# Optimization experiments

Measured on AMD Instinct MI355X. Metric: run time of the kernel, lower is better.

## Reference

```python
import jax, jax.numpy as jnp
import numpy as np

# Model hyperparameters (upscaled from the repo's shakespear config)
L, E, H, T, B, V = 6, 1024, 16, 1024, 4, 32000
HD = E // H          # head_size = 64
EPS = 1e-5


def layernorm(x, g, b):
    m = x.mean(-1, keepdims=True)
    v = ((x - m) ** 2).mean(-1, keepdims=True)
    return (x - m) / jnp.sqrt(v + EPS) * g + b


def setup_inputs() -> dict:
    key = jax.random.key(0)
    ks = jax.random.split(key, 24)
    s = 0.02
    n = lambda k, shp: (jax.random.normal(k, shp) * s).astype(jnp.float32)
    return {
        "idx": jax.random.randint(ks[0], (B, T), 0, V),
        "tok_emb": n(ks[1], (V, E)),
        "pos_emb": n(ks[2], (T, E)),
        # per-head q/k/v weights stacked: [L, E, H, HD]
        "Wq": n(ks[3], (L, E, H, HD)),
        "Wk": n(ks[4], (L, E, H, HD)),
        "Wv": n(ks[5], (L, E, H, HD)),
        "Wo": n(ks[6], (L, E, E)),
        "bo": jnp.zeros((L, E), jnp.float32),
        "W1": n(ks[7], (L, E, 4 * E)),
        "b1": jnp.zeros((L, 4 * E), jnp.float32),
        "W2": n(ks[8], (L, 4 * E, E)),
        "b2": jnp.zeros((L, E), jnp.float32),
        "ln1_g": jnp.ones((L, E), jnp.float32),
        "ln1_b": jnp.zeros((L, E), jnp.float32),
        "ln2_g": jnp.ones((L, E), jnp.float32),
        "ln2_b": jnp.zeros((L, E), jnp.float32),
        "lnf_g": jnp.ones((E,), jnp.float32),
        "lnf_b": jnp.zeros((E,), jnp.float32),
        "Wlm": n(ks[9], (E, V)),
        "blm": jnp.zeros((V,), jnp.float32),
    }


def reference(idx, tok_emb, pos_emb, Wq, Wk, Wv, Wo, bo, W1, b1, W2, b2,
              ln1_g, ln1_b, ln2_g, ln2_b, lnf_g, lnf_b, Wlm, blm):
    x = tok_emb[idx] + pos_emb[None, :T]            # [B,T,E]
    mask = jnp.tril(jnp.ones((T, T), bool))
    scale = HD ** -0.5
    for l in range(L):
        h = layernorm(x, ln1_g[l], ln1_b[l])
        q = jnp.einsum('bte,ehd->bhtd', h, Wq[l])
        k = jnp.einsum('bte,ehd->bhtd', h, Wk[l])
        v = jnp.einsum('bte,ehd->bhtd', h, Wv[l])
        # NOTE: source computes K @ Q^T (reversed from standard attention)
        wei = jnp.einsum('bhtd,bhsd->bhts', k, q) * scale
        wei = jnp.where(mask, wei, -jnp.inf)
        wei = jax.nn.softmax(wei, axis=-1)
        att = jnp.einsum('bhts,bhsd->bhtd', wei, v)  # [B,H,T,HD]
        att = att.transpose(0, 2, 1, 3).reshape(B, T, E)
        x = x + att @ Wo[l] + bo[l]
        h2 = layernorm(x, ln2_g[l], ln2_b[l])
        x = x + jax.nn.relu(h2 @ W1[l] + b1[l]) @ W2[l] + b2[l]
    x = layernorm(x, lnf_g, lnf_b)
    logits = x @ Wlm + blm                           # [B,T,V]
    return logits
```

## Files before the change

kernel.cpp:

```cpp
#include <hip/hip_runtime.h>


typedef __bf16 bf16;
typedef __attribute__((ext_vector_type(8))) __bf16 bf16x8;
typedef __attribute__((ext_vector_type(4))) __bf16 bf16x4;
typedef __attribute__((ext_vector_type(4))) float  f32x4;

#define LAYERS 6
#define EMB    1024
#define HEADS  16
#define HDIM   64
#define SEQ    1024
#define BATCH  4
#define VOCAB  32000
#define ROWS   (BATCH * SEQ)

#define AS1(p) ((__attribute__((address_space(1))) void*)(p))
#define AS3(p) ((__attribute__((address_space(3))) void*)(p))

__global__ void transpose_cvt(const float* __restrict__ in, bf16* __restrict__ out,
                              int K, int N)
{
    __shared__ float tile[32][33];
    int n0 = blockIdx.x * 32, k0 = blockIdx.y * 32;
    int tx = threadIdx.x, ty = threadIdx.y;
#pragma unroll
    for (int r = 0; r < 4; ++r)
        tile[ty + 8 * r][tx] = in[(size_t)(k0 + ty + 8 * r) * N + n0 + tx];
    __syncthreads();
#pragma unroll
    for (int r = 0; r < 4; ++r)
        out[(size_t)(n0 + ty + 8 * r) * K + k0 + tx] = (bf16)tile[tx][ty + 8 * r];
}

__global__ void transpose_all(const float* __restrict__ Wq, const float* __restrict__ Wk,
                              const float* __restrict__ Wv, const float* __restrict__ Wo,
                              const float* __restrict__ W1, const float* __restrict__ W2,
                              bf16* __restrict__ Tq, bf16* __restrict__ Tk,
                              bf16* __restrict__ Tv, bf16* __restrict__ To,
                              bf16* __restrict__ T1, bf16* __restrict__ T2)
{
    __shared__ float tile[32][33];
    int tx = threadIdx.x, ty = threadIdx.y;
    int id = blockIdx.x;
    const float* in; bf16* out; int K, N, n0, k0;
    if (id < 4096) {
        int z = id >> 10, rem = id & 1023;
        int bx = rem & 31, by = rem >> 5;
        K = 1024; N = 1024; n0 = bx * 32; k0 = by * 32;
        switch (z) {
            case 0: in = Wq; out = Tq; break;
            case 1: in = Wk; out = Tk; break;
            case 2: in = Wv; out = Tv; break;
            default: in = Wo; out = To; break;
        }
    } else if (id < 8192) {
        int rem = id - 4096;
        int bx = rem & 127, by = rem >> 7;
        in = W1; out = T1; K = 1024; N = 4096; n0 = bx * 32; k0 = by * 32;
    } else {
        int rem = id - 8192;
        int bx = rem & 127, by = rem >> 7;
        in = W2; out = T2; K = 4096; N = 1024; n0 = by * 32; k0 = bx * 32;
    }
#pragma unroll
    for (int r = 0; r < 4; ++r)
        tile[ty + 8 * r][tx] = in[(size_t)(k0 + ty + 8 * r) * N + n0 + tx];
    __syncthreads();
#pragma unroll
    for (int r = 0; r < 4; ++r)
        out[(size_t)(n0 + ty + 8 * r) * K + k0 + tx] = (bf16)tile[tx][ty + 8 * r];
}

__global__ void embed_kernel(const int* __restrict__ idx, const float* __restrict__ tok,
                             const float* __restrict__ pos, bf16* __restrict__ x)
{
    int row = blockIdx.x;
    int t   = row & (SEQ - 1);
    int id  = idx[row];
    int e   = threadIdx.x;
    float4 a = ((const float4*)(tok + (size_t)id * EMB))[e];
    float4 p = ((const float4*)(pos + (size_t)t  * EMB))[e];
    bf16x4 o;
    o.x = (bf16)(a.x + p.x); o.y = (bf16)(a.y + p.y);
    o.z = (bf16)(a.z + p.z); o.w = (bf16)(a.w + p.w);
    *(bf16x4*)(x + (size_t)row * EMB + e * 4) = o;
}

__global__ __launch_bounds__(256)
void ln_kernel(const bf16* __restrict__ x, const float* __restrict__ g,
               const float* __restrict__ b, bf16* __restrict__ out)
{
    int row = blockIdx.x;
    int t = threadIdx.x;
    bf16x4 xv = *(const bf16x4*)(x + (size_t)row * EMB + t * 4);
    float4 v; v.x = (float)xv.x; v.y = (float)xv.y; v.z = (float)xv.z; v.w = (float)xv.w;
    float s1 = v.x + v.y + v.z + v.w;
    float s2 = v.x * v.x + v.y * v.y + v.z * v.z + v.w * v.w;
#pragma unroll
    for (int off = 32; off > 0; off >>= 1) {
        s1 += __shfl_down(s1, off);
        s2 += __shfl_down(s2, off);
    }
    __shared__ float l1[4], l2[4];
    int wave = t >> 6;
    if ((t & 63) == 0) { l1[wave] = s1; l2[wave] = s2; }
    __syncthreads();
    float tot1 = l1[0] + l1[1] + l1[2] + l1[3];
    float tot2 = l2[0] + l2[1] + l2[2] + l2[3];
    float mean = tot1 * (1.f / EMB);
    float var  = tot2 * (1.f / EMB) - mean * mean;
    float rstd = rsqrtf(var + 1e-5f);
    float4 gg = ((const float4*)g)[t];
    float4 bb = ((const float4*)b)[t];
    bf16x4 o;
    o.x = (bf16)((v.x - mean) * rstd * gg.x + bb.x);
    o.y = (bf16)((v.y - mean) * rstd * gg.y + bb.y);
    o.z = (bf16)((v.z - mean) * rstd * gg.z + bb.z);
    o.w = (bf16)((v.w - mean) * rstd * gg.w + bb.w);
    *(bf16x4*)(out + (size_t)row * EMB + t * 4) = o;
}

template <int MODE>
__global__ __launch_bounds__(512, 1)
void gemm256_kernel(const bf16* __restrict__ A, const bf16* __restrict__ BT,
                    void* Cv, const float* __restrict__ bias,
                    int N, int K, int nbm, int nbn)
{
    __shared__ __align__(16) bf16 lds[2][2][256 * 64];
    const int tid  = threadIdx.x;
    const int wave = tid >> 6, lane = tid & 63;
    const int lo = lane & 15, hi = lane >> 4;
    const int wm = wave >> 2, wn = wave & 3;

    const int nwg = nbm * nbn;
    const int q = nwg >> 3, rem = nwg & 7;
    const int xcd = blockIdx.x & 7, boff = blockIdx.x >> 3;
    const int swz = (xcd < rem ? xcd * (q + 1) : rem * (q + 1) + (xcd - rem) * q) + boff;
    const int m0 = (swz % nbm) * 256;
    const int n0 = (swz / nbm) * 256;

    f32x4 acc[8][4];
#pragma unroll
    for (int m = 0; m < 8; ++m)
#pragma unroll
        for (int n = 0; n < 4; ++n)
            acc[m][n] = (f32x4){0.f, 0.f, 0.f, 0.f};

    const int NT = K >> 6;

    auto stage_ht = [&](int t, int ht) {
        const int slot = t & 1;
        const int k0 = t << 6;
        const int ab = ht >> 1;
        const int rbase = (ht & 1) << 7;
        const bf16* src = ab ? BT : A;
        const int base0 = ab ? n0 : m0;
#pragma unroll
        for (int j = 0; j < 2; ++j) {
            int g  = j * 512 + tid;
            int r  = g >> 3;
            int cc = (g & 7) ^ (r & 7);
            __builtin_amdgcn_global_load_lds(
                AS1(src + (size_t)(base0 + rbase + r) * K + k0 + cc * 8),
                AS3((char*)&lds[slot][ab][rbase * 64] + (size_t)g * 16), 16, 0, 0);
        }
    };

    bf16x8 bcur[4][2], bnxt[4][2], ae[2][2], ao[2][2];

    auto lda = [&](int t, int mp, bf16x8 (&out)[2][2]) {
        const int slot = t & 1;
#pragma unroll
        for (int mi = 0; mi < 2; ++mi)
#pragma unroll
            for (int ks = 0; ks < 2; ++ks) {
                int r = wm * 128 + (mp * 2 + mi) * 16 + lo;
                int pos = (ks * 4 + hi) ^ (r & 7);
                out[mi][ks] = *(const bf16x8*)(&lds[slot][0][r * 64 + pos * 8]);
            }
    };
    auto ldb = [&](int t, bf16x8 (&out)[4][2]) {
        const int slot = t & 1;
#pragma unroll
        for (int n = 0; n < 4; ++n)
#pragma unroll
            for (int ks = 0; ks < 2; ++ks) {
                int r = wn * 64 + n * 16 + lo;
                int pos = (ks * 4 + hi) ^ (r & 7);
                out[n][ks] = *(const bf16x8*)(&lds[slot][1][r * 64 + pos * 8]);
            }
    };
    auto mfma16 = [&](int mp, bf16x8 (&a)[2][2]) {
        __builtin_amdgcn_s_setprio(1);
#pragma unroll
        for (int mi = 0; mi < 2; ++mi)
#pragma unroll
            for (int n = 0; n < 4; ++n)
#pragma unroll
                for (int ks = 0; ks < 2; ++ks)
                    acc[mp * 2 + mi][n] =
                        __builtin_amdgcn_mfma_f32_16x16x32_bf16(a[mi][ks], bcur[n][ks],
                                                                acc[mp * 2 + mi][n], 0, 0, 0);
        __builtin_amdgcn_s_setprio(0);
    };

    stage_ht(0, 0); stage_ht(0, 1); stage_ht(0, 2); stage_ht(0, 3);
    asm volatile("s_waitcnt vmcnt(0)\n\ts_barrier" ::: "memory");
    ldb(0, bcur);
    lda(0, 0, ae);

    for (int t = 0; t < NT; ++t) {
        const bool more = (t + 1 < NT);
        if (more) { stage_ht(t + 1, 0); stage_ht(t + 1, 1); }
        lda(t, 1, ao);
        mfma16(0, ae);
        if (more) { stage_ht(t + 1, 2); stage_ht(t + 1, 3); }
        lda(t, 2, ae);
        mfma16(1, ao);
        lda(t, 3, ao);
        mfma16(2, ae);
        if (more) {
            asm volatile("s_waitcnt vmcnt(0) lgkmcnt(0)\n\ts_barrier" ::: "memory");
            ldb(t + 1, bnxt);
            lda(t + 1, 0, ae);
        }
        mfma16(3, ao);
        if (more) {
#pragma unroll
            for (int n = 0; n < 4; ++n)
#pragma unroll
                for (int ks = 0; ks < 2; ++ks)
                    bcur[n][ks] = bnxt[n][ks];
        }
    }

#pragma unroll
    for (int m = 0; m < 8; ++m) {
        int row = m0 + wm * 128 + m * 16 + hi * 4;
#pragma unroll
        for (int n = 0; n < 4; ++n) {
            int col = n0 + wn * 64 + n * 16 + lo;
            float bv = (MODE != 0) ? bias[col] : 0.f;
#pragma unroll
            for (int j = 0; j < 4; ++j) {
                size_t o = (size_t)(row + j) * N + col;
                float v = acc[m][n][j] + bv;
                if (MODE == 2)      ((bf16*)Cv)[o]  = (bf16)fmaxf(v, 0.f);
                else if (MODE == 3) ((float*)Cv)[o] = v;
                else                ((bf16*)Cv)[o]  = (bf16)v;
            }
        }
    }
}

template <int MODE>
__global__ __launch_bounds__(256)
void gemm_kernel(const bf16* __restrict__ A, const bf16* __restrict__ BT,
                 void* Cv, const float* __restrict__ bias,
                 const bf16* __restrict__ resid, bf16* __restrict__ vt,
                 int N, int K)
{
    __shared__ __align__(16) bf16 As[128 * 64];
    __shared__ __align__(16) bf16 Bs[128 * 64];
    const int tid = threadIdx.x;
    const int wave = tid >> 6, lane = tid & 63;
    const int lo = lane & 15, hi = lane >> 4;
    const int wm = wave >> 1, wn = wave & 1;
    const int m0 = blockIdx.y * 128, n0 = blockIdx.x * 128;

    f32x4 acc[4][4];
#pragma unroll
    for (int m = 0; m < 4; ++m)
#pragma unroll
        for (int n = 0; n < 4; ++n)
            acc[m][n] = (f32x4){0.f, 0.f, 0.f, 0.f};

    const int sb = wave * 4;
    for (int k0 = 0; k0 < K; k0 += 64) {
#pragma unroll
        for (int i = 0; i < 4; ++i) {
            int g   = (sb + i) * 64 + lane;
            int row = g >> 3;
            int lc  = (g & 7) ^ (row & 7);
            const bf16* ga = A  + (size_t)(m0 + row) * K + k0 + lc * 8;
            const bf16* gb = BT + (size_t)(n0 + row) * K + k0 + lc * 8;
            __builtin_amdgcn_global_load_lds(AS1(ga), AS3(As + (sb + i) * 512), 16, 0, 0);
            __builtin_amdgcn_global_load_lds(AS1(gb), AS3(Bs + (sb + i) * 512), 16, 0, 0);
        }
        asm volatile("s_waitcnt vmcnt(0)" ::: "memory");
        __syncthreads();
#pragma unroll
        for (int ks = 0; ks < 2; ++ks) {
            bf16x8 af[4], bfr[4];
#pragma unroll
            for (int m = 0; m < 4; ++m) {
                int r  = wm * 64 + m * 16 + lo;
                int pc = (ks * 4 + hi) ^ (r & 7);
                af[m] = *(const bf16x8*)(As + r * 64 + pc * 8);
            }
#pragma unroll
            for (int n = 0; n < 4; ++n) {
                int r  = wn * 64 + n * 16 + lo;
                int pc = (ks * 4 + hi) ^ (r & 7);
                bfr[n] = *(const bf16x8*)(Bs + r * 64 + pc * 8);
            }
#pragma unroll
            for (int m = 0; m < 4; ++m)
#pragma unroll
                for (int n = 0; n < 4; ++n)
                    acc[m][n] = __builtin_amdgcn_mfma_f32_16x16x32_bf16(af[m], bfr[n], acc[m][n], 0, 0, 0);
        }
        __syncthreads();
    }

    if (MODE == 4 && n0 >= 2048) {
#pragma unroll
        for (int m = 0; m < 4; ++m) {
            int rowb = m0 + wm * 64 + m * 16 + hi * 4;
            int bb = rowb >> 10, t = rowb & 1023;
#pragma unroll
            for (int n = 0; n < 4; ++n) {
                int hd = n0 - 2048 + wn * 64 + n * 16 + lo;
                bf16x4 w;
                w.x = (bf16)acc[m][n][0]; w.y = (bf16)acc[m][n][1];
                w.z = (bf16)acc[m][n][2]; w.w = (bf16)acc[m][n][3];
                *(bf16x4*)(vt + ((size_t)(bb * 1024 + hd)) * SEQ + t) = w;
            }
        }
        return;
    }

#pragma unroll
    for (int m = 0; m < 4; ++m) {
        int rbase = m0 + wm * 64 + m * 16 + hi * 4;
#pragma unroll
        for (int n = 0; n < 4; ++n) {
            int col = n0 + wn * 64 + n * 16 + lo;
            float bv = (MODE == 1) ? bias[col] : 0.f;
#pragma unroll
            for (int j = 0; j < 4; ++j) {
                size_t off = (size_t)(rbase + j) * N + col;
                float v = acc[m][n][j] + bv;
                if (MODE == 1)      ((bf16*)Cv)[off] = (bf16)(v + (float)resid[off]);
                else                ((bf16*)Cv)[off] = (bf16)v;
            }
        }
    }
}

template <int MODE>
__global__ __launch_bounds__(256)
void gemm64_kernel(const bf16* __restrict__ A, const bf16* __restrict__ BT,
                   bf16* __restrict__ C, const float* __restrict__ bias,
                   const bf16* __restrict__ resid, int N, int K)
{
    __shared__ __align__(16) bf16 As[64 * 64];
    __shared__ __align__(16) bf16 Bs[128 * 64];
    const int tid = threadIdx.x;
    const int wave = tid >> 6, lane = tid & 63;
    const int lo = lane & 15, hi = lane >> 4;
    const int wm = wave >> 1, wn = wave & 1;
    const int m0 = blockIdx.y * 64, n0 = blockIdx.x * 128;

    f32x4 acc[2][4];
#pragma unroll
    for (int m = 0; m < 2; ++m)
#pragma unroll
        for (int n = 0; n < 4; ++n)
            acc[m][n] = (f32x4){0.f, 0.f, 0.f, 0.f};

    for (int k0 = 0; k0 < K; k0 += 64) {
#pragma unroll
        for (int i = 0; i < 2; ++i) {
            int c   = i * 256 + tid;
            int row = c >> 3;
            int cc  = (c & 7) ^ (row & 7);
            __builtin_amdgcn_global_load_lds(
                AS1(A + (size_t)(m0 + row) * K + k0 + cc * 8),
                AS3(As + (size_t)c * 8), 16, 0, 0);
        }
#pragma unroll
        for (int i = 0; i < 4; ++i) {
            int c   = i * 256 + tid;
            int row = c >> 3;
            int cc  = (c & 7) ^ (row & 7);
            __builtin_amdgcn_global_load_lds(
                AS1(BT + (size_t)(n0 + row) * K + k0 + cc * 8),
                AS3(Bs + (size_t)c * 8), 16, 0, 0);
        }
        asm volatile("s_waitcnt vmcnt(0)" ::: "memory");
        __syncthreads();
#pragma unroll
        for (int ks = 0; ks < 2; ++ks) {
            bf16x8 af[2], bfr[4];
#pragma unroll
            for (int m = 0; m < 2; ++m) {
                int r  = wm * 32 + m * 16 + lo;
                int pc = (ks * 4 + hi) ^ (r & 7);
                af[m] = *(const bf16x8*)(As + r * 64 + pc * 8);
            }
#pragma unroll
            for (int n = 0; n < 4; ++n) {
                int r  = wn * 64 + n * 16 + lo;
                int pc = (ks * 4 + hi) ^ (r & 7);
                bfr[n] = *(const bf16x8*)(Bs + r * 64 + pc * 8);
            }
#pragma unroll
            for (int m = 0; m < 2; ++m)
#pragma unroll
                for (int n = 0; n < 4; ++n)
                    acc[m][n] = __builtin_amdgcn_mfma_f32_16x16x32_bf16(af[m], bfr[n], acc[m][n], 0, 0, 0);
        }
        __syncthreads();
    }

#pragma unroll
    for (int m = 0; m < 2; ++m) {
        int rbase = m0 + wm * 32 + m * 16 + hi * 4;
#pragma unroll
        for (int n = 0; n < 4; ++n) {
            int col = n0 + wn * 64 + n * 16 + lo;
            float bv = bias[col];
#pragma unroll
            for (int j = 0; j < 4; ++j) {
                size_t off = (size_t)(rbase + j) * N + col;
                float v = acc[m][n][j] + bv;
                if (MODE == 1) C[off] = (bf16)(v + (float)resid[off]);
                else           C[off] = (bf16)fmaxf(v, 0.f);
            }
        }
    }
}

__global__ __launch_bounds__(64)
void attn_kernel(const bf16* __restrict__ qkv, const bf16* __restrict__ vt,
                 bf16* __restrict__ att)
{
    int bh = blockIdx.x; int b = bh >> 4, h = bh & 15;
    int t0 = blockIdx.y * 16;
    int lane = threadIdx.x;
    int lo = lane & 15, hi = lane >> 4;
    const bf16* kb = qkv + (size_t)(b * SEQ) * 3072 + EMB + h * 64;
    const bf16* qb = qkv + (size_t)(b * SEQ) * 3072 + h * 64;
    const bf16* vb = vt + (size_t)bh * 64 * SEQ;

    bf16x8 bK0 = *(const bf16x8*)(kb + (size_t)(t0 + lo) * 3072 + hi * 8);
    bf16x8 bK1 = *(const bf16x8*)(kb + (size_t)(t0 + lo) * 3072 + 32 + hi * 8);

    f32x4 o[4];
#pragma unroll
    for (int n = 0; n < 4; ++n) o[n] = (f32x4){0.f, 0.f, 0.f, 0.f};
    float mrun = -1e30f, lrun = 0.f;

    __shared__ __align__(16) bf16 plds[16][72];

    const int nt = (t0 + 16 + 63) >> 6;
    const int nfull = (t0 >= 64) ? (((t0 - 63) >> 6) + 1) : 0;

    auto tile_body = [&](int s0, bool masked) {
        f32x4 sc[4];
#pragma unroll
        for (int sh = 0; sh < 4; ++sh) sc[sh] = (f32x4){0.f, 0.f, 0.f, 0.f};
#pragma unroll
        for (int sh = 0; sh < 4; ++sh) {
            const bf16* qr = qb + (size_t)(s0 + sh * 16 + lo) * 3072;
            bf16x8 aQ0 = *(const bf16x8*)(qr + hi * 8);
            bf16x8 aQ1 = *(const bf16x8*)(qr + 32 + hi * 8);
            sc[sh] = __builtin_amdgcn_mfma_f32_16x16x32_bf16(aQ0, bK0, sc[sh], 0, 0, 0);
            sc[sh] = __builtin_amdgcn_mfma_f32_16x16x32_bf16(aQ1, bK1, sc[sh], 0, 0, 0);
        }
        const int tt = t0 + lo;
        float p[16];
        float mx = -1e30f;
#pragma unroll
        for (int sh = 0; sh < 4; ++sh)
#pragma unroll
            for (int j = 0; j < 4; ++j) {
                float val = sc[sh][j] * 0.125f;
                if (masked) {
                    int s = s0 + sh * 16 + hi * 4 + j;
                    if (s > tt) val = -1e30f;
                }
                p[sh * 4 + j] = val;
                mx = fmaxf(mx, val);
            }
        mx = fmaxf(mx, __shfl_xor(mx, 16));
        mx = fmaxf(mx, __shfl_xor(mx, 32));
        if (__any(mx > mrun + 8.f)) {
            float mnew = fmaxf(mrun, mx);
            float scl = __expf(mrun - mnew);
            mrun = mnew;
            lrun *= scl;
            float sclj[4];
#pragma unroll
            for (int j = 0; j < 4; ++j) sclj[j] = __shfl(scl, hi * 4 + j);
#pragma unroll
            for (int n = 0; n < 4; ++n)
#pragma unroll
                for (int j = 0; j < 4; ++j)
                    o[n][j] *= sclj[j];
        }
        float rs = 0.f;
#pragma unroll
        for (int i = 0; i < 16; ++i) { p[i] = __expf(p[i] - mrun); rs += p[i]; }
        rs += __shfl_xor(rs, 16);
        rs += __shfl_xor(rs, 32);
        lrun += rs;
        __syncthreads();
#pragma unroll
        for (int sh = 0; sh < 4; ++sh) {
            bf16x4 w;
            w.x = (bf16)p[sh * 4 + 0]; w.y = (bf16)p[sh * 4 + 1];
            w.z = (bf16)p[sh * 4 + 2]; w.w = (bf16)p[sh * 4 + 3];
            *(bf16x4*)(&plds[lo][sh * 16 + hi * 4]) = w;
        }
        __syncthreads();
        bf16x8 aP0 = *(const bf16x8*)(&plds[lo][hi * 8]);
        bf16x8 aP1 = *(const bf16x8*)(&plds[lo][32 + hi * 8]);
#pragma unroll
        for (int n = 0; n < 4; ++n) {
            bf16x8 bV0 = *(const bf16x8*)(vb + (size_t)(n * 16 + lo) * SEQ + s0 + hi * 8);
            bf16x8 bV1 = *(const bf16x8*)(vb + (size_t)(n * 16 + lo) * SEQ + s0 + 32 + hi * 8);
            o[n] = __builtin_amdgcn_mfma_f32_16x16x32_bf16(aP0, bV0, o[n], 0, 0, 0);
            o[n] = __builtin_amdgcn_mfma_f32_16x16x32_bf16(aP1, bV1, o[n], 0, 0, 0);
        }
    };

    for (int it = 0; it < nfull; ++it) tile_body(it * 64, false);
    for (int it = nfull; it < nt; ++it) tile_body(it * 64, true);

    float lj[4];
#pragma unroll
    for (int j = 0; j < 4; ++j) lj[j] = __shfl(lrun, hi * 4 + j);
#pragma unroll
    for (int j = 0; j < 4; ++j) {
        float inv = 1.f / lj[j];
        size_t rowoff = (size_t)(b * SEQ + t0 + hi * 4 + j) * EMB + h * 64;
#pragma unroll
        for (int n = 0; n < 4; ++n)
            att[rowoff + n * 16 + lo] = (bf16)(o[n][j] * inv);
    }
}

extern "C" void kernel_launch(void* const* d_in, const int* in_sizes, int n_in,
                              void* d_out, int out_size, void* d_ws, size_t ws_size,
                              hipStream_t stream)
{
    const int*   idx  = (const int*)d_in[0];
    const float* tok  = (const float*)d_in[1];
    const float* pos  = (const float*)d_in[2];
    const float* Wq   = (const float*)d_in[3];
    const float* Wk   = (const float*)d_in[4];
    const float* Wv   = (const float*)d_in[5];
    const float* Wo   = (const float*)d_in[6];
    const float* bo   = (const float*)d_in[7];
    const float* W1   = (const float*)d_in[8];
    const float* b1   = (const float*)d_in[9];
    const float* W2   = (const float*)d_in[10];
    const float* b2   = (const float*)d_in[11];
    const float* ln1g = (const float*)d_in[12];
    const float* ln1b = (const float*)d_in[13];
    const float* ln2g = (const float*)d_in[14];
    const float* ln2b = (const float*)d_in[15];
    const float* lnfg = (const float*)d_in[16];
    const float* lnfb = (const float*)d_in[17];
    const float* Wlm  = (const float*)d_in[18];
    const float* blm  = (const float*)d_in[19];
    float* out = (float*)d_out;

    char* ws = (char*)d_ws;
    size_t off = 0;
    auto alloc = [&](size_t bytes) { void* p = ws + off; off += (bytes + 255) & ~(size_t)255; return p; };
    bf16* x     = (bf16*)alloc((size_t)ROWS * EMB * 2);
    bf16* h     = (bf16*)alloc((size_t)ROWS * EMB * 2);
    bf16* qkv   = (bf16*)alloc((size_t)ROWS * 3072 * 2);
    bf16* vt    = (bf16*)alloc((size_t)ROWS * EMB * 2);
    bf16* attb  = (bf16*)alloc((size_t)ROWS * EMB * 2);
    bf16* mlp   = (bf16*)alloc((size_t)ROWS * 4096 * 2);
    bf16* WTqkv = (bf16*)alloc((size_t)3072 * 1024 * 2);
    bf16* WTo   = (bf16*)alloc((size_t)1024 * 1024 * 2);
    bf16* WT1   = (bf16*)alloc((size_t)4096 * 1024 * 2);
    bf16* WT2   = (bf16*)alloc((size_t)1024 * 4096 * 2);
    bf16* WTlm  = (bf16*)alloc((size_t)VOCAB * 1024 * 2);

    dim3 tb(32, 8);

    transpose_cvt<<<dim3(VOCAB / 32, 32), tb, 0, stream>>>(Wlm, WTlm, 1024, VOCAB);

    embed_kernel<<<ROWS, 256, 0, stream>>>(idx, tok, pos, x);

    for (int l = 0; l < LAYERS; ++l) {
        const size_t wqs = (size_t)l * 1024 * 1024;
        const size_t w14 = (size_t)l * 4096 * 1024;
        transpose_all<<<12288, tb, 0, stream>>>(
            Wq + wqs, Wk + wqs, Wv + wqs, Wo + wqs, W1 + w14, W2 + w14,
            WTqkv, WTqkv + (size_t)1024 * 1024, WTqkv + (size_t)2048 * 1024, WTo,
            WT1, WT2);

        ln_kernel<<<ROWS, 256, 0, stream>>>(x, ln1g + l * EMB, ln1b + l * EMB, h);
        gemm_kernel<4><<<dim3(24, 32), 256, 0, stream>>>(h, WTqkv, qkv, nullptr, nullptr, vt, 3072, 1024);
        attn_kernel<<<dim3(64, 64), 64, 0, stream>>>(qkv, vt, attb);
        gemm64_kernel<1><<<dim3(8, 64), 256, 0, stream>>>(attb, WTo, x, bo + l * EMB, x, 1024, 1024);
        ln_kernel<<<ROWS, 256, 0, stream>>>(x, ln2g + l * EMB, ln2b + l * EMB, h);
        gemm64_kernel<2><<<dim3(32, 64), 256, 0, stream>>>(h, WT1, mlp, b1 + l * 4096, nullptr, 4096, 1024);
        gemm64_kernel<1><<<dim3(8, 64), 256, 0, stream>>>(mlp, WT2, x, b2 + l * EMB, x, 1024, 4096);
    }
    ln_kernel<<<ROWS, 256, 0, stream>>>(x, lnfg, lnfb, h);
    gemm256_kernel<3><<<16 * 125, 512, 0, stream>>>(h, WTlm, out, blm, 32000, 1024, 16, 125);
}
```

Measured before the change: 1.910 ms.

## Process 32 query rows per attention wave and use 256-tile GEMM for MLP up-projection

The attention kernel now handles two 16-row groups per 64-thread block, so each loaded Q tile and V tile feeds twice as many MFMAs, and the grid is halved. The online-softmax rescale check is merged across both groups. Separately, the W1 MLP GEMM moves from the 64-tile kernel to the larger 256-tile kernel, which gives more operand reuse per block. The costs are higher register pressure in attention, fewer blocks for latency hiding, and only 256 blocks for the MLP GEMM.

```diff
diff --git a/kernel.cpp b/kernel.cpp
--- a/kernel.cpp
+++ b/kernel.cpp
@@ -438,108 +438,140 @@
                  bf16* __restrict__ att)
 {
     int bh = blockIdx.x; int b = bh >> 4, h = bh & 15;
-    int t0 = blockIdx.y * 16;
+    int t0 = blockIdx.y * 32;
     int lane = threadIdx.x;
     int lo = lane & 15, hi = lane >> 4;
     const bf16* kb = qkv + (size_t)(b * SEQ) * 3072 + EMB + h * 64;
     const bf16* qb = qkv + (size_t)(b * SEQ) * 3072 + h * 64;
     const bf16* vb = vt + (size_t)bh * 64 * SEQ;
 
-    bf16x8 bK0 = *(const bf16x8*)(kb + (size_t)(t0 + lo) * 3072 + hi * 8);
-    bf16x8 bK1 = *(const bf16x8*)(kb + (size_t)(t0 + lo) * 3072 + 32 + hi * 8);
-
-    f32x4 o[4];
-#pragma unroll
-    for (int n = 0; n < 4; ++n) o[n] = (f32x4){0.f, 0.f, 0.f, 0.f};
-    float mrun = -1e30f, lrun = 0.f;
-
-    __shared__ __align__(16) bf16 plds[16][72];
-
-    const int nt = (t0 + 16 + 63) >> 6;
+    bf16x8 bK[2][2];
+#pragma unroll
+    for (int g = 0; g < 2; ++g) {
+        bK[g][0] = *(const bf16x8*)(kb + (size_t)(t0 + g * 16 + lo) * 3072 + hi * 8);
+        bK[g][1] = *(const bf16x8*)(kb + (size_t)(t0 + g * 16 + lo) * 3072 + 32 + hi * 8);
+    }
+
+    f32x4 o[2][4];
+#pragma unroll
+    for (int g = 0; g < 2; ++g)
+#pragma unroll
+        for (int n = 0; n < 4; ++n) o[g][n] = (f32x4){0.f, 0.f, 0.f, 0.f};
+    float mrun[2] = {-1e30f, -1e30f}, lrun[2] = {0.f, 0.f};
+
+    __shared__ __align__(16) bf16 plds[32][72];
+
+    const int nt = (t0 + 32 + 63) >> 6;
     const int nfull = (t0 >= 64) ? (((t0 - 63) >> 6) + 1) : 0;
 
     auto tile_body = [&](int s0, bool masked) {
-        f32x4 sc[4];
-#pragma unroll
-        for (int sh = 0; sh < 4; ++sh) sc[sh] = (f32x4){0.f, 0.f, 0.f, 0.f};
+        f32x4 sc[2][4];
+#pragma unroll
+        for (int g = 0; g < 2; ++g)
+#pragma unroll
+            for (int sh = 0; sh < 4; ++sh) sc[g][sh] = (f32x4){0.f, 0.f, 0.f, 0.f};
 #pragma unroll
         for (int sh = 0; sh < 4; ++sh) {
             const bf16* qr = qb + (size_t)(s0 + sh * 16 + lo) * 3072;
             bf16x8 aQ0 = *(const bf16x8*)(qr + hi * 8);
             bf16x8 aQ1 = *(const bf16x8*)(qr + 32 + hi * 8);
-            sc[sh] = __builtin_amdgcn_mfma_f32_16x16x32_bf16(aQ0, bK0, sc[sh], 0, 0, 0);
-            sc[sh] = __builtin_amdgcn_mfma_f32_16x16x32_bf16(aQ1, bK1, sc[sh], 0, 0, 0);
-        }
-        const int tt = t0 + lo;
-        float p[16];
-        float mx = -1e30f;
-#pragma unroll
-        for (int sh = 0; sh < 4; ++sh)
-#pragma unroll
-            for (int j = 0; j < 4; ++j) {
-                float val = sc[sh][j] * 0.125f;
-                if (masked) {
-                    int s = s0 + sh * 16 + hi * 4 + j;
-                    if (s > tt) val = -1e30f;
+#pragma unroll
+            for (int g = 0; g < 2; ++g) {
+                sc[g][sh] = __builtin_amdgcn_mfma_f32_16x16x32_bf16(aQ0, bK[g][0], sc[g][sh], 0, 0, 0);
+                sc[g][sh] = __builtin_amdgcn_mfma_f32_16x16x32_bf16(aQ1, bK[g][1], sc[g][sh], 0, 0, 0);
+            }
+        }
+        float p[2][16], mx[2];
+#pragma unroll
+        for (int g = 0; g < 2; ++g) {
+            const int tt = t0 + g * 16 + lo;
+            mx[g] = -1e30f;
+#pragma unroll
+            for (int sh = 0; sh < 4; ++sh)
+#pragma unroll
+                for (int j = 0; j < 4; ++j) {
+                    float val = sc[g][sh][j] * 0.125f;
+                    if (masked) {
+                        int s = s0 + sh * 16 + hi * 4 + j;
+                        if (s > tt) val = -1e30f;
+                    }
+                    p[g][sh * 4 + j] = val;
+                    mx[g] = fmaxf(mx[g], val);
                 }
-                p[sh * 4 + j] = val;
-                mx = fmaxf(mx, val);
-            }
-        mx = fmaxf(mx, __shfl_xor(mx, 16));
-        mx = fmaxf(mx, __shfl_xor(mx, 32));
-        if (__any(mx > mrun + 8.f)) {
-            float mnew = fmaxf(mrun, mx);
-            float scl = __expf(mrun - mnew);
-            mrun = mnew;
-            lrun *= scl;
-            float sclj[4];
-#pragma unroll
-            for (int j = 0; j < 4; ++j) sclj[j] = __shfl(scl, hi * 4 + j);
-#pragma unroll
-            for (int n = 0; n < 4; ++n)
-#pragma unroll
-                for (int j = 0; j < 4; ++j)
-                    o[n][j] *= sclj[j];
-        }
-        float rs = 0.f;
-#pragma unroll
-        for (int i = 0; i < 16; ++i) { p[i] = __expf(p[i] - mrun); rs += p[i]; }
-        rs += __shfl_xor(rs, 16);
-        rs += __shfl_xor(rs, 32);
-        lrun += rs;
+            mx[g] = fmaxf(mx[g], __shfl_xor(mx[g], 16));
+            mx[g] = fmaxf(mx[g], __shfl_xor(mx[g], 32));
+        }
+        if (__any(fmaxf(mx[0] - mrun[0], mx[1] - mrun[1]) > 8.f)) {
+#pragma unroll
+            for (int g = 0; g < 2; ++g) {
+                float mnew = fmaxf(mrun[g], mx[g]);
+                float scl = __expf(mrun[g] - mnew);
+                mrun[g] = mnew;
+                lrun[g] *= scl;
+                float sclj[4];
+#pragma unroll
+                for (int j = 0; j < 4; ++j) sclj[j] = __shfl(scl, hi * 4 + j);
+#pragma unroll
+                for (int n = 0; n < 4; ++n)
+#pragma unroll
+                    for (int j = 0; j < 4; ++j)
+                        o[g][n][j] *= sclj[j];
+            }
+        }
+#pragma unroll
+        for (int g = 0; g < 2; ++g) {
+            float rs = 0.f;
+#pragma unroll
+            for (int i = 0; i < 16; ++i) { p[g][i] = __expf(p[g][i] - mrun[g]); rs += p[g][i]; }
+            rs += __shfl_xor(rs, 16);
+            rs += __shfl_xor(rs, 32);
+            lrun[g] += rs;
+        }
         __syncthreads();
 #pragma unroll
-        for (int sh = 0; sh < 4; ++sh) {
-            bf16x4 w;
-            w.x = (bf16)p[sh * 4 + 0]; w.y = (bf16)p[sh * 4 + 1];
-            w.z = (bf16)p[sh * 4 + 2]; w.w = (bf16)p[sh * 4 + 3];
-            *(bf16x4*)(&plds[lo][sh * 16 + hi * 4]) = w;
-        }
+        for (int g = 0; g < 2; ++g)
+#pragma unroll
+            for (int sh = 0; sh < 4; ++sh) {
+                bf16x4 w;
+                w.x = (bf16)p[g][sh * 4 + 0]; w.y = (bf16)p[g][sh * 4 + 1];
+                w.z = (bf16)p[g][sh * 4 + 2]; w.w = (bf16)p[g][sh * 4 + 3];
+                *(bf16x4*)(&plds[g * 16 + lo][sh * 16 + hi * 4]) = w;
+            }
         __syncthreads();
-        bf16x8 aP0 = *(const bf16x8*)(&plds[lo][hi * 8]);
-        bf16x8 aP1 = *(const bf16x8*)(&plds[lo][32 + hi * 8]);
+        bf16x8 aP[2][2];
+#pragma unroll
+        for (int g = 0; g < 2; ++g) {
+            aP[g][0] = *(const bf16x8*)(&plds[g * 16 + lo][hi * 8]);
+            aP[g][1] = *(const bf16x8*)(&plds[g * 16 + lo][32 + hi * 8]);
+        }
 #pragma unroll
         for (int n = 0; n < 4; ++n) {
             bf16x8 bV0 = *(const bf16x8*)(vb + (size_t)(n * 16 + lo) * SEQ + s0 + hi * 8);
             bf16x8 bV1 = *(const bf16x8*)(vb + (size_t)(n * 16 + lo) * SEQ + s0 + 32 + hi * 8);
-            o[n] = __builtin_amdgcn_mfma_f32_16x16x32_bf16(aP0, bV0, o[n], 0, 0, 0);
-            o[n] = __builtin_amdgcn_mfma_f32_16x16x32_bf16(aP1, bV1, o[n], 0, 0, 0);
+#pragma unroll
+            for (int g = 0; g < 2; ++g) {
+                o[g][n] = __builtin_amdgcn_mfma_f32_16x16x32_bf16(aP[g][0], bV0, o[g][n], 0, 0, 0);
+                o[g][n] = __builtin_amdgcn_mfma_f32_16x16x32_bf16(aP[g][1], bV1, o[g][n], 0, 0, 0);
+            }
         }
     };
 
     for (int it = 0; it < nfull; ++it) tile_body(it * 64, false);
     for (int it = nfull; it < nt; ++it) tile_body(it * 64, true);
 
-    float lj[4];
-#pragma unroll
-    for (int j = 0; j < 4; ++j) lj[j] = __shfl(lrun, hi * 4 + j);
-#pragma unroll
-    for (int j = 0; j < 4; ++j) {
-        float inv = 1.f / lj[j];
-        size_t rowoff = (size_t)(b * SEQ + t0 + hi * 4 + j) * EMB + h * 64;
-#pragma unroll
-        for (int n = 0; n < 4; ++n)
-            att[rowoff + n * 16 + lo] = (bf16)(o[n][j] * inv);
+#pragma unroll
+    for (int g = 0; g < 2; ++g) {
+        float lj[4];
+#pragma unroll
+        for (int j = 0; j < 4; ++j) lj[j] = __shfl(lrun[g], hi * 4 + j);
+#pragma unroll
+        for (int j = 0; j < 4; ++j) {
+            float inv = 1.f / lj[j];
+            size_t rowoff = (size_t)(b * SEQ + t0 + g * 16 + hi * 4 + j) * EMB + h * 64;
+#pragma unroll
+            for (int n = 0; n < 4; ++n)
+                att[rowoff + n * 16 + lo] = (bf16)(o[g][n][j] * inv);
+        }
     }
 }
 
@@ -600,10 +632,10 @@
 
         ln_kernel<<<ROWS, 256, 0, stream>>>(x, ln1g + l * EMB, ln1b + l * EMB, h);
         gemm_kernel<4><<<dim3(24, 32), 256, 0, stream>>>(h, WTqkv, qkv, nullptr, nullptr, vt, 3072, 1024);
-        attn_kernel<<<dim3(64, 64), 64, 0, stream>>>(qkv, vt, attb);
+        attn_kernel<<<dim3(64, 32), 64, 0, stream>>>(qkv, vt, attb);
         gemm64_kernel<1><<<dim3(8, 64), 256, 0, stream>>>(attb, WTo, x, bo + l * EMB, x, 1024, 1024);
         ln_kernel<<<ROWS, 256, 0, stream>>>(x, ln2g + l * EMB, ln2b + l * EMB, h);
-        gemm64_kernel<2><<<dim3(32, 64), 256, 0, stream>>>(h, WT1, mlp, b1 + l * 4096, nullptr, 4096, 1024);
+        gemm256_kernel<2><<<16 * 16, 512, 0, stream>>>(h, WT1, mlp, b1 + l * 4096, 4096, 1024, 16, 16);
         gemm64_kernel<1><<<dim3(8, 64), 256, 0, stream>>>(mlp, WT2, x, b2 + l * EMB, x, 1024, 4096);
     }
     ln_kernel<<<ROWS, 256, 0, stream>>>(x, lnfg, lnfb, h);
```

Result: faster. 1.748 ms (-8.5%).
